# Kernel tuning notes

Measured on AMD Instinct MI355X. Metric: run time of the kernel, lower is better.

Reference implementation:

```python
import jax, jax.numpy as jnp
import numpy as np

N = 8192
IN_F = 512
OUT_F = 512


def setup_inputs() -> dict:
    key = jax.random.key(0)
    k1, k2, k3, k4, k5 = jax.random.split(key, 5)
    scale = 1.0 / np.sqrt(IN_F)
    return {
        "embedding": jax.random.normal(k1, (N, IN_F), dtype=jnp.float32),
        "W_qk": jax.random.uniform(k2, (OUT_F, IN_F), dtype=jnp.float32, minval=-scale, maxval=scale),
        "b_qk": jax.random.uniform(k3, (OUT_F,), dtype=jnp.float32, minval=-scale, maxval=scale),
        "W_v": jax.random.uniform(k4, (OUT_F, IN_F), dtype=jnp.float32, minval=-scale, maxval=scale),
        "b_v": jax.random.uniform(k5, (OUT_F,), dtype=jnp.float32, minval=-scale, maxval=scale),
    }


def reference(embedding, W_qk, b_qk, W_v, b_v):
    # Q and K share the same projection (query_key Linear)
    Q = embedding @ W_qk.T + b_qk          # [N, D]
    K = Q                                   # identical projection
    V = embedding @ W_v.T + b_v             # [N, D]
    inv_sqrt_d = 1.0 / jnp.sqrt(jnp.asarray(OUT_F, dtype=embedding.dtype))
    scores = (Q @ K.T) * inv_sqrt_d         # [N, N]
    attn = jax.nn.softmax(scores, axis=1)   # row-wise softmax (dim=1)
    return attn @ V                         # [N, D]
```

## Files before the change

### kernel.cpp

```cpp
#include <hip/hip_runtime.h>
#include <hip/hip_bf16.h>


#define NTOK 8192
#define DIM  512

typedef unsigned short ushort_t;
typedef __attribute__((ext_vector_type(8))) __bf16 bf16x8;
typedef __attribute__((ext_vector_type(4))) float f32x4;

__device__ __forceinline__ float bf2f(ushort_t u) {
    union { unsigned int i; float f; } v; v.i = ((unsigned int)u) << 16; return v.f;
}
__device__ __forceinline__ ushort_t f2bf(float f) {
    union { float f; unsigned int i; } v; v.f = f;
    unsigned int b = v.i;
    return (ushort_t)((b + 0x7FFFu + ((b >> 16) & 1u)) >> 16);
}
__device__ __forceinline__ __bf16 f2bfh(float f) {
    union { ushort_t u; __bf16 h; } c; c.u = f2bf(f); return c.h;
}
__device__ __forceinline__ f32x4 mfma16(bf16x8 a, bf16x8 b, f32x4 c) {
    return __builtin_amdgcn_mfma_f32_16x16x32_bf16(a, b, c, 0, 0, 0);
}
__device__ __forceinline__ bf16x8 load8(const void* p, size_t idx, bool f32) {
    if (f32) {
        const float* f = (const float*)p + idx;
        bf16x8 r;
        #pragma unroll
        for (int j = 0; j < 8; ++j) r[j] = f2bfh(f[j]);
        return r;
    }
    return *(const bf16x8*)((const ushort_t*)p + idx);
}
__device__ __forceinline__ float loadS(const void* p, size_t idx, bool f32) {
    return f32 ? ((const float*)p)[idx] : bf2f(((const ushort_t*)p)[idx]);
}

#define LDA 520
#define LDP 264

__global__ void detect_kernel(const ushort_t* __restrict__ emb, int* __restrict__ flag)
{
    int lane = threadIdx.x;
    int cnt = 0;
    #pragma unroll
    for (int i = 0; i < 8; ++i) {
        ushort_t u = emb[(size_t)(lane * 8 + i) * 2];
        int a = u & 0x7FFF;
        int e = (u >> 7) & 0xFF;
        if (a == 0 || (e >= 111 && e <= 143)) cnt++;
    }
    cnt += __shfl_xor(cnt, 1);  cnt += __shfl_xor(cnt, 2);  cnt += __shfl_xor(cnt, 4);
    cnt += __shfl_xor(cnt, 8);  cnt += __shfl_xor(cnt, 16); cnt += __shfl_xor(cnt, 32);
    if (lane == 0) *flag = (cnt >= 460) ? 1 : 0;
}

__global__ __launch_bounds__(256)
void prep_kernel(const int* __restrict__ flag,
                 const void* __restrict__ Wqk, const void* __restrict__ bqk,
                 const void* __restrict__ Wv,  const void* __restrict__ bv,
                 ushort_t* __restrict__ Wqkb, ushort_t* __restrict__ bqkb,
                 ushort_t* __restrict__ Wvb,  ushort_t* __restrict__ bvb)
{
    const bool f32 = (*flag == 0);
    size_t gid = (size_t)blockIdx.x * 256 + threadIdx.x;
    size_t base = gid * 8;
    *(bf16x8*)&Wqkb[base] = load8(Wqk, base, f32);
    *(bf16x8*)&Wvb[base]  = load8(Wv,  base, f32);
    if (gid < 64) {
        *(bf16x8*)&bqkb[base] = load8(bqk, base, f32);
        *(bf16x8*)&bvb[base]  = load8(bv,  base, f32);
    }
}

__global__ __launch_bounds__(512)
void projqT_kernel(const int* __restrict__ flag, const void* __restrict__ emb,
                   const ushort_t* __restrict__ Wb, const ushort_t* __restrict__ bb,
                   ushort_t* __restrict__ C, ushort_t* __restrict__ embT)
{
    __shared__ ushort_t Alds[64][LDA];
    const bool f32 = (*flag == 0);
    const int tid  = threadIdx.x;
    const int wave = tid >> 6;
    const int lane = tid & 63;
    const int quad = lane >> 4;
    const int col  = lane & 15;
    const int mblk = blockIdx.x * 64;

    #pragma unroll
    for (int i = 0; i < 8; ++i) {
        int chunk = i * 512 + tid;
        int row = chunk >> 6;
        int k8  = (chunk & 63) * 8;
        *(bf16x8*)&Alds[row][k8] = load8(emb, (size_t)(mblk + row) * 512 + k8, f32);
    }
    __syncthreads();

    {
        ushort_t buf[64];
        #pragma unroll
        for (int r = 0; r < 64; ++r) buf[r] = Alds[r][tid];
        ushort_t* dst = embT + (size_t)tid * NTOK + mblk;
        #pragma unroll
        for (int i = 0; i < 8; ++i)
            *(uint4*)(dst + i * 8) = *(uint4*)&buf[i * 8];
    }

    f32x4 acc[4][4];
    #pragma unroll
    for (int r = 0; r < 4; ++r)
        #pragma unroll
        for (int c = 0; c < 4; ++c) acc[r][c] = (f32x4){0.f, 0.f, 0.f, 0.f};

    const int wcol = wave * 64;
    #pragma unroll
    for (int kk = 0; kk < 16; ++kk) {
        bf16x8 a[4];
        #pragma unroll
        for (int r = 0; r < 4; ++r)
            a[r] = *(const bf16x8*)&Alds[r * 16 + col][kk * 32 + quad * 8];
        #pragma unroll
        for (int c = 0; c < 4; ++c) {
            bf16x8 b = *(const bf16x8*)&Wb[(size_t)(wcol + c * 16 + col) * 512
                                           + kk * 32 + quad * 8];
            #pragma unroll
            for (int r = 0; r < 4; ++r)
                acc[r][c] = mfma16(a[r], b, acc[r][c]);
        }
    }

    #pragma unroll
    for (int r = 0; r < 4; ++r)
        #pragma unroll
        for (int c = 0; c < 4; ++c)
            #pragma unroll
            for (int g = 0; g < 4; ++g) {
                int m = mblk + r * 16 + quad * 4 + g;
                int n = wcol + c * 16 + col;
                C[(size_t)m * DIM + n] = f2bf(acc[r][c][g] + bf2f(bb[n]));
            }
}

__global__ __launch_bounds__(1024)
void attn64_kernel(const ushort_t* __restrict__ Q, const ushort_t* __restrict__ embT,
                   ushort_t* __restrict__ P0, ushort_t* __restrict__ P1,
                   float* __restrict__ lsumA)
{
    __shared__ ushort_t Qlds[64][LDA];
    __shared__ ushort_t Plds[2][64][LDP];
    __shared__ float    Lp[16][64];

    const int tid  = threadIdx.x;
    const int wave = tid >> 6;
    const int lane = tid & 63;
    const int quad = lane >> 4;
    const int col  = lane & 15;
    const int qt   = blockIdx.x & 127;
    const int ks   = blockIdx.x >> 7;
    const int q0   = qt * 64;
    const int kbase = ks * 4096;
    ushort_t* Ps = ks ? P1 : P0;

    #pragma unroll
    for (int i = 0; i < 4; ++i) {
        int chunk = i * 1024 + tid;
        int row = chunk >> 6;
        int k8  = (chunk & 63) * 8;
        *(bf16x8*)&Qlds[row][k8] = *(const bf16x8*)&Q[(size_t)(q0 + row) * 512 + k8];
    }
    __syncthreads();

    f32x4 accO[4][2];
    #pragma unroll
    for (int r = 0; r < 4; ++r)
        #pragma unroll
        for (int c = 0; c < 2; ++c) accO[r][c] = (f32x4){0.f, 0.f, 0.f, 0.f};

    float lsum[4][4];
    #pragma unroll
    for (int r = 0; r < 4; ++r)
        #pragma unroll
        for (int g = 0; g < 4; ++g) lsum[r][g] = 0.f;

    const float sc = 0.04419417382415922f * 1.4426950408889634f;
    const int wd = wave * 32;

    for (int it = 0; it < 16; ++it) {
        const int j0  = kbase + it * 256;
        const int buf = it & 1;

        f32x4 accS[4];
        #pragma unroll
        for (int r = 0; r < 4; ++r) accS[r] = (f32x4){0.f, 0.f, 0.f, 0.f};
        const size_t keyrow = (size_t)(j0 + wave * 16 + col) * 512;
        #pragma unroll
        for (int h = 0; h < 2; ++h) {
            bf16x8 kb[8];
            #pragma unroll
            for (int kk = 0; kk < 8; ++kk)
                kb[kk] = *(const bf16x8*)&Q[keyrow + (h * 8 + kk) * 32 + quad * 8];
            #pragma unroll
            for (int kk = 0; kk < 8; ++kk) {
                const int cofs = (h * 8 + kk) * 32 + quad * 8;
                #pragma unroll
                for (int r = 0; r < 4; ++r) {
                    bf16x8 a = *(const bf16x8*)&Qlds[r * 16 + col][cofs];
                    accS[r] = mfma16(a, kb[kk], accS[r]);
                }
            }
        }

        bf16x8 vbA[8];
        #pragma unroll
        for (int kk = 0; kk < 4; ++kk)
            #pragma unroll
            for (int c = 0; c < 2; ++c)
                vbA[kk * 2 + c] = *(const bf16x8*)&embT[
                    (size_t)(wd + c * 16 + col) * NTOK + j0 + kk * 32 + quad * 8];

        #pragma unroll
        for (int r = 0; r < 4; ++r)
            #pragma unroll
            for (int g = 0; g < 4; ++g) {
                float p = exp2f(fminf(accS[r][g] * sc, 126.0f));
                lsum[r][g] += p;
                Plds[buf][r * 16 + quad * 4 + g][wave * 16 + col] = f2bf(p);
            }

        bf16x8 vbB[8];
        #pragma unroll
        for (int kk = 0; kk < 4; ++kk)
            #pragma unroll
            for (int c = 0; c < 2; ++c)
                vbB[kk * 2 + c] = *(const bf16x8*)&embT[
                    (size_t)(wd + c * 16 + col) * NTOK + j0 + (4 + kk) * 32 + quad * 8];

        __syncthreads();

        #pragma unroll
        for (int kk = 0; kk < 4; ++kk) {
            #pragma unroll
            for (int r = 0; r < 4; ++r) {
                bf16x8 a = *(const bf16x8*)&Plds[buf][r * 16 + col][kk * 32 + quad * 8];
                #pragma unroll
                for (int c = 0; c < 2; ++c)
                    accO[r][c] = mfma16(a, vbA[kk * 2 + c], accO[r][c]);
            }
        }
        #pragma unroll
        for (int kk = 0; kk < 4; ++kk) {
            #pragma unroll
            for (int r = 0; r < 4; ++r) {
                bf16x8 a = *(const bf16x8*)&Plds[buf][r * 16 + col][(4 + kk) * 32 + quad * 8];
                #pragma unroll
                for (int c = 0; c < 2; ++c)
                    accO[r][c] = mfma16(a, vbB[kk * 2 + c], accO[r][c]);
            }
        }
    }

    #pragma unroll
    for (int r = 0; r < 4; ++r)
        #pragma unroll
        for (int g = 0; g < 4; ++g) {
            float s = lsum[r][g];
            s += __shfl_xor(s, 1);
            s += __shfl_xor(s, 2);
            s += __shfl_xor(s, 4);
            s += __shfl_xor(s, 8);
            if (col == 0)
                Lp[wave][r * 16 + quad * 4 + g] = s;
        }
    __syncthreads();
    if (tid < 64) {
        float t = 0.f;
        #pragma unroll
        for (int w = 0; w < 16; ++w) t += Lp[w][tid];
        lsumA[(size_t)ks * NTOK + q0 + tid] = t;
    }

    #pragma unroll
    for (int r = 0; r < 4; ++r)
        #pragma unroll
        for (int c = 0; c < 2; ++c)
            #pragma unroll
            for (int g = 0; g < 4; ++g)
                Ps[(size_t)(q0 + r * 16 + quad * 4 + g) * DIM + wd + c * 16 + col]
                    = f2bf(accO[r][c][g]);
}

__global__ __launch_bounds__(512)
void finalize_kernel(const int* __restrict__ flag,
                     const ushort_t* __restrict__ P0, const ushort_t* __restrict__ P1,
                     const float* __restrict__ lsumA,
                     const ushort_t* __restrict__ Wb, const ushort_t* __restrict__ bb,
                     void* __restrict__ Out)
{
    __shared__ ushort_t Alds[64][LDA];
    const bool f32 = (*flag == 0);
    const int tid  = threadIdx.x;
    const int wave = tid >> 6;
    const int lane = tid & 63;
    const int quad = lane >> 4;
    const int col  = lane & 15;
    const int mblk = blockIdx.x * 64;

    #pragma unroll
    for (int i = 0; i < 8; ++i) {
        int chunk = i * 512 + tid;
        int row = chunk >> 6;
        int k8  = (chunk & 63) * 8;
        int m   = mblk + row;
        float rv = 1.0f / (lsumA[m] + lsumA[NTOK + m]);
        bf16x8 v0 = *(const bf16x8*)&P0[(size_t)m * 512 + k8];
        bf16x8 v1 = *(const bf16x8*)&P1[(size_t)m * 512 + k8];
        bf16x8 t;
        #pragma unroll
        for (int j = 0; j < 8; ++j) t[j] = f2bfh(((float)v0[j] + (float)v1[j]) * rv);
        *(bf16x8*)&Alds[row][k8] = t;
    }
    __syncthreads();

    f32x4 acc[4][4];
    #pragma unroll
    for (int r = 0; r < 4; ++r)
        #pragma unroll
        for (int c = 0; c < 4; ++c) acc[r][c] = (f32x4){0.f, 0.f, 0.f, 0.f};

    const int wcol = wave * 64;
    #pragma unroll
    for (int kk = 0; kk < 16; ++kk) {
        bf16x8 a[4];
        #pragma unroll
        for (int r = 0; r < 4; ++r)
            a[r] = *(const bf16x8*)&Alds[r * 16 + col][kk * 32 + quad * 8];
        #pragma unroll
        for (int c = 0; c < 4; ++c) {
            bf16x8 b = *(const bf16x8*)&Wb[(size_t)(wcol + c * 16 + col) * 512
                                           + kk * 32 + quad * 8];
            #pragma unroll
            for (int r = 0; r < 4; ++r)
                acc[r][c] = mfma16(a[r], b, acc[r][c]);
        }
    }

    #pragma unroll
    for (int r = 0; r < 4; ++r)
        #pragma unroll
        for (int c = 0; c < 4; ++c)
            #pragma unroll
            for (int g = 0; g < 4; ++g) {
                int m = mblk + r * 16 + quad * 4 + g;
                int n = wcol + c * 16 + col;
                float v = acc[r][c][g] + bf2f(bb[n]);
                if (f32) ((float*)Out)[(size_t)m * DIM + n] = v;
                else     ((ushort_t*)Out)[(size_t)m * DIM + n] = f2bf(v);
            }
}

__global__ __launch_bounds__(256)
void transpose_kernel(const int* __restrict__ flag, const void* __restrict__ emb,
                      ushort_t* __restrict__ embT)
{
    __shared__ float tile[64][65];
    const bool f32 = (*flag == 0);
    const int t  = threadIdx.x;
    const int j0 = blockIdx.x * 64;
    const int d0 = blockIdx.y * 64;
    {
        int r = t >> 2, cs = (t & 3) * 16;
        if (f32) {
            const float* src = (const float*)emb + (size_t)(j0 + r) * DIM + d0 + cs;
            #pragma unroll
            for (int i = 0; i < 16; i += 4) {
                float4 v = *(const float4*)(src + i);
                tile[r][cs + i]     = v.x;
                tile[r][cs + i + 1] = v.y;
                tile[r][cs + i + 2] = v.z;
                tile[r][cs + i + 3] = v.w;
            }
        } else {
            const ushort_t* src = (const ushort_t*)emb + (size_t)(j0 + r) * DIM + d0 + cs;
            #pragma unroll
            for (int i = 0; i < 16; ++i) tile[r][cs + i] = bf2f(src[i]);
        }
    }
    __syncthreads();
    {
        int d = t >> 2, js = (t & 3) * 16;
        ushort_t buf[16];
        #pragma unroll
        for (int i = 0; i < 16; ++i) buf[i] = f2bf(tile[js + i][d]);
        ushort_t* dst = embT + (size_t)(d0 + d) * NTOK + j0 + js;
        *(uint4*)dst       = *(uint4*)&buf[0];
        *(uint4*)(dst + 8) = *(uint4*)&buf[8];
    }
}

__global__ __launch_bounds__(512)
void projq_kernel(const int* __restrict__ flag, const void* __restrict__ emb,
                  const void* __restrict__ W, const void* __restrict__ bias,
                  ushort_t* __restrict__ C)
{
    __shared__ ushort_t Alds[32][LDA];
    const bool f32 = (*flag == 0);
    const int tid  = threadIdx.x;
    const int wave = tid >> 6;
    const int lane = tid & 63;
    const int quad = lane >> 4;
    const int col  = lane & 15;
    const int mblk = blockIdx.x * 32;

    #pragma unroll
    for (int i = 0; i < 4; ++i) {
        int chunk = i * 512 + tid;
        int row = chunk >> 6;
        int k8  = (chunk & 63) * 8;
        *(bf16x8*)&Alds[row][k8] = load8(emb, (size_t)(mblk + row) * 512 + k8, f32);
    }
    __syncthreads();

    f32x4 acc[2][4];
    #pragma unroll
    for (int r = 0; r < 2; ++r)
        #pragma unroll
        for (int c = 0; c < 4; ++c) acc[r][c] = (f32x4){0.f, 0.f, 0.f, 0.f};

    const int wcol = wave * 64;
    #pragma unroll
    for (int kk = 0; kk < 16; ++kk) {
        bf16x8 a0 = *(const bf16x8*)&Alds[col][kk * 32 + quad * 8];
        bf16x8 a1 = *(const bf16x8*)&Alds[16 + col][kk * 32 + quad * 8];
        #pragma unroll
        for (int c = 0; c < 4; ++c) {
            bf16x8 b = load8(W, (size_t)(wcol + c * 16 + col) * 512 + kk * 32 + quad * 8, f32);
            acc[0][c] = mfma16(a0, b, acc[0][c]);
            acc[1][c] = mfma16(a1, b, acc[1][c]);
        }
    }

    #pragma unroll
    for (int r = 0; r < 2; ++r)
        #pragma unroll
        for (int c = 0; c < 4; ++c)
            #pragma unroll
            for (int g = 0; g < 4; ++g) {
                int m = mblk + r * 16 + quad * 4 + g;
                int n = wcol + c * 16 + col;
                C[(size_t)m * DIM + n] = f2bf(acc[r][c][g] + loadS(bias, n, f32));
            }
}

template <int VT>
__global__ __launch_bounds__(1024)
void attn_fused_kernel(const int* __restrict__ flag, const ushort_t* __restrict__ Q,
                       const void* __restrict__ embOrT, const void* __restrict__ Wv,
                       const void* __restrict__ bv, void* __restrict__ Out)
{
    __shared__ ushort_t Qlds[32][LDA];
    __shared__ ushort_t Plds[2][32][LDP];
    __shared__ float    Lpart[16][32];

    const bool f32 = (*flag == 0);
    const int tid  = threadIdx.x;
    const int wave = tid >> 6;
    const int lane = tid & 63;
    const int quad = lane >> 4;
    const int col  = lane & 15;
    const int q0   = blockIdx.x * 32;

    #pragma unroll
    for (int i = 0; i < 2; ++i) {
        int chunk = i * 1024 + tid;
        int row = chunk >> 6;
        int k8  = (chunk & 63) * 8;
        *(bf16x8*)&Qlds[row][k8] = *(const bf16x8*)&Q[(size_t)(q0 + row) * 512 + k8];
    }
    __syncthreads();

    f32x4 accO[2][2];
    #pragma unroll
    for (int r = 0; r < 2; ++r)
        #pragma unroll
        for (int c = 0; c < 2; ++c) accO[r][c] = (f32x4){0.f, 0.f, 0.f, 0.f};

    float lsum[2][4];
    #pragma unroll
    for (int r = 0; r < 2; ++r)
        #pragma unroll
        for (int g = 0; g < 4; ++g) lsum[r][g] = 0.f;

    const float sc = 0.04419417382415922f * 1.4426950408889634f;
    const int wOcol = wave * 32;

    for (int it = 0; it < 32; ++it) {
        const int j0  = it * 256;
        const int buf = it & 1;

        bf16x8 kb[16];
        const size_t keyrow = (size_t)(j0 + wave * 16 + col) * 512;
        #pragma unroll
        for (int kk = 0; kk < 16; ++kk)
            kb[kk] = *(const bf16x8*)&Q[keyrow + kk * 32 + quad * 8];

        f32x4 accS[2];
        accS[0] = (f32x4){0.f, 0.f, 0.f, 0.f};
        accS[1] = (f32x4){0.f, 0.f, 0.f, 0.f};
        #pragma unroll
        for (int kk = 0; kk < 16; ++kk) {
            bf16x8 a0 = *(const bf16x8*)&Qlds[col][kk * 32 + quad * 8];
            bf16x8 a1 = *(const bf16x8*)&Qlds[16 + col][kk * 32 + quad * 8];
            accS[0] = mfma16(a0, kb[kk], accS[0]);
            accS[1] = mfma16(a1, kb[kk], accS[1]);
        }

        bf16x8 vb[16];
        #pragma unroll
        for (int kk = 0; kk < 8; ++kk)
            #pragma unroll
            for (int c = 0; c < 2; ++c) {
                if (VT) {
                    vb[kk * 2 + c] = *(const bf16x8*)((const ushort_t*)embOrT
                        + (size_t)(wOcol + c * 16 + col) * NTOK + j0 + kk * 32 + quad * 8);
                } else {
                    size_t base = (size_t)(j0 + kk * 32 + quad * 8) * 512 + (wOcol + c * 16 + col);
                    bf16x8 b;
                    if (f32) {
                        const float* bp = (const float*)embOrT + base;
                        #pragma unroll
                        for (int j = 0; j < 8; ++j) b[j] = f2bfh(bp[(size_t)j * 512]);
                    } else {
                        const __bf16* bp = (const __bf16*)embOrT + base;
                        #pragma unroll
                        for (int j = 0; j < 8; ++j) b[j] = bp[(size_t)j * 512];
                    }
                    vb[kk * 2 + c] = b;
                }
            }

        #pragma unroll
        for (int r = 0; r < 2; ++r)
            #pragma unroll
            for (int g = 0; g < 4; ++g) {
                float p = exp2f(fminf(accS[r][g] * sc, 126.0f));
                lsum[r][g] += p;
                Plds[buf][r * 16 + quad * 4 + g][wave * 16 + col] = f2bf(p);
            }

        __syncthreads();

        #pragma unroll
        for (int kk = 0; kk < 8; ++kk) {
            bf16x8 a0 = *(const bf16x8*)&Plds[buf][col][kk * 32 + quad * 8];
            bf16x8 a1 = *(const bf16x8*)&Plds[buf][16 + col][kk * 32 + quad * 8];
            #pragma unroll
            for (int c = 0; c < 2; ++c) {
                accO[0][c] = mfma16(a0, vb[kk * 2 + c], accO[0][c]);
                accO[1][c] = mfma16(a1, vb[kk * 2 + c], accO[1][c]);
            }
        }
    }

    #pragma unroll
    for (int r = 0; r < 2; ++r)
        #pragma unroll
        for (int g = 0; g < 4; ++g) {
            float s = lsum[r][g];
            s += __shfl_xor(s, 1);
            s += __shfl_xor(s, 2);
            s += __shfl_xor(s, 4);
            s += __shfl_xor(s, 8);
            lsum[r][g] = s;
        }
    if (col == 0) {
        #pragma unroll
        for (int r = 0; r < 2; ++r)
            #pragma unroll
            for (int g = 0; g < 4; ++g)
                Lpart[wave][r * 16 + quad * 4 + g] = lsum[r][g];
    }
    __syncthreads();

    #pragma unroll
    for (int r = 0; r < 2; ++r) {
        float rinv[4];
        #pragma unroll
        for (int g = 0; g < 4; ++g) {
            float t = 0.f;
            #pragma unroll
            for (int w = 0; w < 16; ++w) t += Lpart[w][r * 16 + quad * 4 + g];
            rinv[g] = 1.0f / t;
        }
        #pragma unroll
        for (int c = 0; c < 2; ++c)
            #pragma unroll
            for (int g = 0; g < 4; ++g)
                Qlds[r * 16 + quad * 4 + g][wOcol + c * 16 + col] = f2bf(accO[r][c][g] * rinv[g]);
    }
    __syncthreads();

    f32x4 acc2[2][2];
    #pragma unroll
    for (int r = 0; r < 2; ++r)
        #pragma unroll
        for (int c = 0; c < 2; ++c) acc2[r][c] = (f32x4){0.f, 0.f, 0.f, 0.f};

    #pragma unroll
    for (int kk = 0; kk < 16; ++kk) {
        bf16x8 a0 = *(const bf16x8*)&Qlds[col][kk * 32 + quad * 8];
        bf16x8 a1 = *(const bf16x8*)&Qlds[16 + col][kk * 32 + quad * 8];
        #pragma unroll
        for (int c = 0; c < 2; ++c) {
            bf16x8 b = load8(Wv, (size_t)(wOcol + c * 16 + col) * 512 + kk * 32 + quad * 8, f32);
            acc2[0][c] = mfma16(a0, b, acc2[0][c]);
            acc2[1][c] = mfma16(a1, b, acc2[1][c]);
        }
    }

    #pragma unroll
    for (int r = 0; r < 2; ++r)
        #pragma unroll
        for (int c = 0; c < 2; ++c)
            #pragma unroll
            for (int g = 0; g < 4; ++g) {
                int m = q0 + r * 16 + quad * 4 + g;
                int n = wOcol + c * 16 + col;
                float v = acc2[r][c][g] + loadS(bv, n, f32);
                if (f32) ((float*)Out)[(size_t)m * DIM + n] = v;
                else     ((ushort_t*)Out)[(size_t)m * DIM + n] = f2bf(v);
            }
}

extern "C" void kernel_launch(void* const* d_in, const int* in_sizes, int n_in,
                              void* d_out, int out_size, void* d_ws, size_t ws_size,
                              hipStream_t stream)
{
    const void* emb = d_in[0];
    const void* Wqk = d_in[1];
    const void* bqk = d_in[2];
    const void* Wv  = d_in[3];
    const void* bv  = d_in[4];

    char* W = (char*)d_ws;
    int*      flag  = (int*)W;
    float*    lsumA = (float*)(W + 64);
    ushort_t* Wqkb  = (ushort_t*)(W + 64 + 65536);
    ushort_t* Wvb   = Wqkb + (size_t)DIM * DIM;
    ushort_t* bqkb  = Wvb + (size_t)DIM * DIM;
    ushort_t* bvb   = bqkb + DIM;
    ushort_t* embT  = bvb + DIM;
    ushort_t* Qws   = embT + (size_t)DIM * NTOK;
    ushort_t* P0    = Qws + (size_t)DIM * NTOK;
    ushort_t* P1    = P0 + (size_t)NTOK * DIM;

    const size_t needA = 64 + 65536 + 2 * (size_t)DIM * DIM * 2 + 2 * DIM * 2
                       + 4 * (size_t)NTOK * DIM * 2;
    const size_t needB = 64 + 2 * (size_t)NTOK * DIM * 2;

    detect_kernel<<<dim3(1), dim3(64), 0, stream>>>((const ushort_t*)emb, flag);

    if (ws_size >= needA) {
        prep_kernel<<<dim3(128), dim3(256), 0, stream>>>(flag, Wqk, bqk, Wv, bv,
                                                         Wqkb, bqkb, Wvb, bvb);
        projqT_kernel<<<dim3(NTOK / 64), dim3(512), 0, stream>>>(flag, emb, Wqkb, bqkb,
                                                                 Qws, embT);
        attn64_kernel<<<dim3(256), dim3(1024), 0, stream>>>(Qws, embT, P0, P1, lsumA);
        finalize_kernel<<<dim3(NTOK / 64), dim3(512), 0, stream>>>(flag, P0, P1, lsumA,
                                                                   Wvb, bvb, d_out);
    } else if (ws_size >= needB) {
        ushort_t* embT2 = (ushort_t*)(W + 64);
        ushort_t* Qws2  = embT2 + (size_t)DIM * NTOK;
        transpose_kernel<<<dim3(128, 8), dim3(256), 0, stream>>>(flag, emb, embT2);
        projq_kernel<<<dim3(NTOK / 32), dim3(512), 0, stream>>>(flag, emb, Wqk, bqk, Qws2);
        attn_fused_kernel<1><<<dim3(NTOK / 32), dim3(1024), 0, stream>>>(
            flag, Qws2, embT2, Wv, bv, d_out);
    } else {
        ushort_t* Qsm = (ushort_t*)(W + 64);
        projq_kernel<<<dim3(NTOK / 32), dim3(512), 0, stream>>>(flag, emb, Wqk, bqk, Qsm);
        attn_fused_kernel<0><<<dim3(NTOK / 32), dim3(1024), 0, stream>>>(
            flag, Qsm, emb, Wv, bv, d_out);
    }
}
```

Baseline: 383.2 us.

## Retile attention to 128-query blocks with 4-way key split and swizzled LDS

Replaces the 64-query, 2-way key-split attention kernel with a 128-query, 4-way key-split kernel of 8 waves, each computing a 64-wide output slice. Q and P tiles in LDS use XOR swizzling to avoid bank conflicts, and P is written in two phases of 64 keys. The larger query tile is meant to halve the K/V global reads per query and raise MFMA reuse. In exchange it needs more registers and LDS per block, adds syncs per iteration, and the finalize step must now sum four partial outputs, which needs more workspace.

```diff
diff --git a/kernel.cpp b/kernel.cpp
--- a/kernel.cpp
+++ b/kernel.cpp
@@ -142,126 +142,126 @@
             }
 }
 
-__global__ __launch_bounds__(1024)
-void attn64_kernel(const ushort_t* __restrict__ Q, const ushort_t* __restrict__ embT,
-                   ushort_t* __restrict__ P0, ushort_t* __restrict__ P1,
-                   float* __restrict__ lsumA)
-{
-    __shared__ ushort_t Qlds[64][LDA];
-    __shared__ ushort_t Plds[2][64][LDP];
-    __shared__ float    Lp[16][64];
+__global__ __launch_bounds__(512)
+void attn128_kernel(const ushort_t* __restrict__ Q, const ushort_t* __restrict__ embT,
+                    ushort_t* __restrict__ Pall, float* __restrict__ lsumA)
+{
+    __shared__ ushort_t Qlds[128 * 512];
+    __shared__ ushort_t Plds[128 * 64];
+    __shared__ float    Lp[8][128];
 
     const int tid  = threadIdx.x;
     const int wave = tid >> 6;
     const int lane = tid & 63;
     const int quad = lane >> 4;
     const int col  = lane & 15;
-    const int qt   = blockIdx.x & 127;
-    const int ks   = blockIdx.x >> 7;
-    const int q0   = qt * 64;
-    const int kbase = ks * 4096;
-    ushort_t* Ps = ks ? P1 : P0;
-
-    #pragma unroll
-    for (int i = 0; i < 4; ++i) {
-        int chunk = i * 1024 + tid;
-        int row = chunk >> 6;
-        int k8  = (chunk & 63) * 8;
-        *(bf16x8*)&Qlds[row][k8] = *(const bf16x8*)&Q[(size_t)(q0 + row) * 512 + k8];
-    }
-    __syncthreads();
-
-    f32x4 accO[4][2];
-    #pragma unroll
-    for (int r = 0; r < 4; ++r)
-        #pragma unroll
-        for (int c = 0; c < 2; ++c) accO[r][c] = (f32x4){0.f, 0.f, 0.f, 0.f};
-
-    float lsum[4][4];
-    #pragma unroll
-    for (int r = 0; r < 4; ++r)
+    const int qt   = blockIdx.x >> 2;
+    const int ks   = blockIdx.x & 3;
+    const int q0   = qt * 128;
+    const int kb0  = ks * 2048;
+    ushort_t* Ps = Pall + (size_t)ks * NTOK * DIM;
+
+    {
+        const int srow = tid >> 2, scb = (tid & 3) * 16;
+        const ushort_t* src = &Q[(size_t)(q0 + srow) * 512];
+        ushort_t* dstrow = &Qlds[srow * 512];
+        const int sw = (srow & 7) * 8;
+        #pragma unroll
+        for (int i = 0; i < 16; ++i) {
+            int c8 = (scb + i) * 8;
+            *(bf16x8*)&dstrow[c8 ^ sw] = *(const bf16x8*)&src[c8];
+        }
+    }
+    __syncthreads();
+
+    f32x4 accO[8][4];
+    #pragma unroll
+    for (int r = 0; r < 8; ++r)
+        #pragma unroll
+        for (int c = 0; c < 4; ++c) accO[r][c] = (f32x4){0.f, 0.f, 0.f, 0.f};
+
+    float lsum[8][4];
+    #pragma unroll
+    for (int r = 0; r < 8; ++r)
         #pragma unroll
         for (int g = 0; g < 4; ++g) lsum[r][g] = 0.f;
 
     const float sc = 0.04419417382415922f * 1.4426950408889634f;
-    const int wd = wave * 32;
+    const int wd = wave * 64;
+    const int colsw = (col & 7) * 8;
 
     for (int it = 0; it < 16; ++it) {
-        const int j0  = kbase + it * 256;
-        const int buf = it & 1;
-
-        f32x4 accS[4];
-        #pragma unroll
-        for (int r = 0; r < 4; ++r) accS[r] = (f32x4){0.f, 0.f, 0.f, 0.f};
+        const int j0 = kb0 + it * 128;
+
+        f32x4 accS[8];
+        #pragma unroll
+        for (int r = 0; r < 8; ++r) accS[r] = (f32x4){0.f, 0.f, 0.f, 0.f};
         const size_t keyrow = (size_t)(j0 + wave * 16 + col) * 512;
         #pragma unroll
-        for (int h = 0; h < 2; ++h) {
-            bf16x8 kb[8];
-            #pragma unroll
-            for (int kk = 0; kk < 8; ++kk)
-                kb[kk] = *(const bf16x8*)&Q[keyrow + (h * 8 + kk) * 32 + quad * 8];
-            #pragma unroll
-            for (int kk = 0; kk < 8; ++kk) {
-                const int cofs = (h * 8 + kk) * 32 + quad * 8;
+        for (int kc2 = 0; kc2 < 8; ++kc2) {
+            bf16x8 kA = *(const bf16x8*)&Q[keyrow + (kc2 * 2) * 32 + quad * 8];
+            bf16x8 kB = *(const bf16x8*)&Q[keyrow + (kc2 * 2 + 1) * 32 + quad * 8];
+            #pragma unroll
+            for (int k = 0; k < 2; ++k) {
+                const int cofs = (kc2 * 2 + k) * 32 + quad * 8;
+                bf16x8 kb8 = k ? kB : kA;
                 #pragma unroll
-                for (int r = 0; r < 4; ++r) {
-                    bf16x8 a = *(const bf16x8*)&Qlds[r * 16 + col][cofs];
-                    accS[r] = mfma16(a, kb[kk], accS[r]);
+                for (int r = 0; r < 8; ++r) {
+                    bf16x8 a = *(const bf16x8*)&Qlds[(r * 16 + col) * 512 + (cofs ^ colsw)];
+                    accS[r] = mfma16(a, kb8, accS[r]);
                 }
             }
         }
 
-        bf16x8 vbA[8];
-        #pragma unroll
-        for (int kk = 0; kk < 4; ++kk)
-            #pragma unroll
-            for (int c = 0; c < 2; ++c)
-                vbA[kk * 2 + c] = *(const bf16x8*)&embT[
-                    (size_t)(wd + c * 16 + col) * NTOK + j0 + kk * 32 + quad * 8];
-
-        #pragma unroll
-        for (int r = 0; r < 4; ++r)
+        #pragma unroll
+        for (int r = 0; r < 8; ++r)
             #pragma unroll
             for (int g = 0; g < 4; ++g) {
-                float p = exp2f(fminf(accS[r][g] * sc, 126.0f));
-                lsum[r][g] += p;
-                Plds[buf][r * 16 + quad * 4 + g][wave * 16 + col] = f2bf(p);
-            }
-
-        bf16x8 vbB[8];
-        #pragma unroll
-        for (int kk = 0; kk < 4; ++kk)
-            #pragma unroll
-            for (int c = 0; c < 2; ++c)
-                vbB[kk * 2 + c] = *(const bf16x8*)&embT[
-                    (size_t)(wd + c * 16 + col) * NTOK + j0 + (4 + kk) * 32 + quad * 8];
-
-        __syncthreads();
-
-        #pragma unroll
-        for (int kk = 0; kk < 4; ++kk) {
-            #pragma unroll
-            for (int r = 0; r < 4; ++r) {
-                bf16x8 a = *(const bf16x8*)&Plds[buf][r * 16 + col][kk * 32 + quad * 8];
+                float v = exp2f(fminf(accS[r][g] * sc, 126.0f));
+                accS[r][g] = v;
+                lsum[r][g] += v;
+            }
+
+        #pragma unroll
+        for (int ph = 0; ph < 2; ++ph) {
+            if ((wave >> 2) == ph) {
+                const int klb = (wave & 3) * 16;
                 #pragma unroll
-                for (int c = 0; c < 2; ++c)
-                    accO[r][c] = mfma16(a, vbA[kk * 2 + c], accO[r][c]);
-            }
-        }
-        #pragma unroll
-        for (int kk = 0; kk < 4; ++kk) {
-            #pragma unroll
-            for (int r = 0; r < 4; ++r) {
-                bf16x8 a = *(const bf16x8*)&Plds[buf][r * 16 + col][(4 + kk) * 32 + quad * 8];
+                for (int r = 0; r < 8; ++r)
+                    #pragma unroll
+                    for (int g = 0; g < 4; ++g) {
+                        int prow = r * 16 + quad * 4 + g;
+                        int kl   = klb + col;
+                        int kch  = kl >> 3;
+                        Plds[prow * 64 + (((kch ^ (prow & 7)) << 3) | (kl & 7))]
+                            = f2bf(accS[r][g]);
+                    }
+            }
+            __syncthreads();
+
+            #pragma unroll
+            for (int kf = 0; kf < 2; ++kf) {
+                const size_t kgl = (size_t)j0 + ph * 64 + kf * 32 + quad * 8;
+                bf16x8 vb[4];
                 #pragma unroll
-                for (int c = 0; c < 2; ++c)
-                    accO[r][c] = mfma16(a, vbB[kk * 2 + c], accO[r][c]);
-            }
-        }
-    }
-
-    #pragma unroll
-    for (int r = 0; r < 4; ++r)
+                for (int c = 0; c < 4; ++c)
+                    vb[c] = *(const bf16x8*)&embT[(size_t)(wd + c * 16 + col) * NTOK + kgl];
+                #pragma unroll
+                for (int r = 0; r < 8; ++r) {
+                    int prow = r * 16 + col;
+                    bf16x8 a = *(const bf16x8*)&Plds[prow * 64
+                                  + (((kf * 4 + quad) ^ (prow & 7)) << 3)];
+                    #pragma unroll
+                    for (int c = 0; c < 4; ++c)
+                        accO[r][c] = mfma16(a, vb[c], accO[r][c]);
+                }
+            }
+            __syncthreads();
+        }
+    }
+
+    #pragma unroll
+    for (int r = 0; r < 8; ++r)
         #pragma unroll
         for (int g = 0; g < 4; ++g) {
             float s = lsum[r][g];
@@ -273,17 +273,17 @@
                 Lp[wave][r * 16 + quad * 4 + g] = s;
         }
     __syncthreads();
-    if (tid < 64) {
+    if (tid < 128) {
         float t = 0.f;
         #pragma unroll
-        for (int w = 0; w < 16; ++w) t += Lp[w][tid];
+        for (int w = 0; w < 8; ++w) t += Lp[w][tid];
         lsumA[(size_t)ks * NTOK + q0 + tid] = t;
     }
 
     #pragma unroll
-    for (int r = 0; r < 4; ++r)
-        #pragma unroll
-        for (int c = 0; c < 2; ++c)
+    for (int r = 0; r < 8; ++r)
+        #pragma unroll
+        for (int c = 0; c < 4; ++c)
             #pragma unroll
             for (int g = 0; g < 4; ++g)
                 Ps[(size_t)(q0 + r * 16 + quad * 4 + g) * DIM + wd + c * 16 + col]
@@ -291,8 +291,7 @@
 }
 
 __global__ __launch_bounds__(512)
-void finalize_kernel(const int* __restrict__ flag,
-                     const ushort_t* __restrict__ P0, const ushort_t* __restrict__ P1,
+void finalize_kernel(const int* __restrict__ flag, const ushort_t* __restrict__ Pall,
                      const float* __restrict__ lsumA,
                      const ushort_t* __restrict__ Wb, const ushort_t* __restrict__ bb,
                      void* __restrict__ Out)
@@ -312,13 +311,21 @@
         int row = chunk >> 6;
         int k8  = (chunk & 63) * 8;
         int m   = mblk + row;
-        float rv = 1.0f / (lsumA[m] + lsumA[NTOK + m]);
-        bf16x8 v0 = *(const bf16x8*)&P0[(size_t)m * 512 + k8];
-        bf16x8 v1 = *(const bf16x8*)&P1[(size_t)m * 512 + k8];
-        bf16x8 t;
-        #pragma unroll
-        for (int j = 0; j < 8; ++j) t[j] = f2bfh(((float)v0[j] + (float)v1[j]) * rv);
-        *(bf16x8*)&Alds[row][k8] = t;
+        float rv = 1.0f / (lsumA[m] + lsumA[NTOK + m] + lsumA[2 * NTOK + m]
+                           + lsumA[3 * NTOK + m]);
+        float s[8];
+        #pragma unroll
+        for (int j = 0; j < 8; ++j) s[j] = 0.f;
+        #pragma unroll
+        for (int t = 0; t < 4; ++t) {
+            bf16x8 v = *(const bf16x8*)&Pall[(size_t)t * NTOK * DIM + (size_t)m * 512 + k8];
+            #pragma unroll
+            for (int j = 0; j < 8; ++j) s[j] += (float)v[j];
+        }
+        bf16x8 o;
+        #pragma unroll
+        for (int j = 0; j < 8; ++j) o[j] = f2bfh(s[j] * rv);
+        *(bf16x8*)&Alds[row][k8] = o;
     }
     __syncthreads();
 
@@ -645,17 +652,16 @@
     char* W = (char*)d_ws;
     int*      flag  = (int*)W;
     float*    lsumA = (float*)(W + 64);
-    ushort_t* Wqkb  = (ushort_t*)(W + 64 + 65536);
+    ushort_t* Wqkb  = (ushort_t*)(W + 64 + 131072);
     ushort_t* Wvb   = Wqkb + (size_t)DIM * DIM;
     ushort_t* bqkb  = Wvb + (size_t)DIM * DIM;
     ushort_t* bvb   = bqkb + DIM;
     ushort_t* embT  = bvb + DIM;
     ushort_t* Qws   = embT + (size_t)DIM * NTOK;
-    ushort_t* P0    = Qws + (size_t)DIM * NTOK;
-    ushort_t* P1    = P0 + (size_t)NTOK * DIM;
-
-    const size_t needA = 64 + 65536 + 2 * (size_t)DIM * DIM * 2 + 2 * DIM * 2
-                       + 4 * (size_t)NTOK * DIM * 2;
+    ushort_t* Pall  = Qws + (size_t)DIM * NTOK;
+
+    const size_t needA = 64 + 131072 + 2 * (size_t)DIM * DIM * 2 + 2 * DIM * 2
+                       + 6 * (size_t)NTOK * DIM * 2;
     const size_t needB = 64 + 2 * (size_t)NTOK * DIM * 2;
 
     detect_kernel<<<dim3(1), dim3(64), 0, stream>>>((const ushort_t*)emb, flag);
@@ -665,9 +671,9 @@
                                                          Wqkb, bqkb, Wvb, bvb);
         projqT_kernel<<<dim3(NTOK / 64), dim3(512), 0, stream>>>(flag, emb, Wqkb, bqkb,
                                                                  Qws, embT);
-        attn64_kernel<<<dim3(256), dim3(1024), 0, stream>>>(Qws, embT, P0, P1, lsumA);
-        finalize_kernel<<<dim3(NTOK / 64), dim3(512), 0, stream>>>(flag, P0, P1, lsumA,
-                                                                   Wvb, bvb, d_out);
+        attn128_kernel<<<dim3(256), dim3(512), 0, stream>>>(Qws, embT, Pall, lsumA);
+        finalize_kernel<<<dim3(NTOK / 64), dim3(512), 0, stream>>>(flag, Pall, lsumA,
+                                                                   Wqkb == nullptr ? nullptr : Wvb, bvb, d_out);
     } else if (ws_size >= needB) {
         ushort_t* embT2 = (ushort_t*)(W + 64);
         ushort_t* Qws2  = embT2 + (size_t)DIM * NTOK;
```

Result: slower. 769.3 us (+100.8%).
